# Performance work log

Hardware: AMD Instinct MI355X
Metric: run time of the kernel (lower is better)

## Reference

```python
import jax, jax.numpy as jnp
import numpy as np
from jax import lax

HID = 96              # hidden_dim (C)
DM  = 2 * HID         # SS2D d_model (real+imag interleaved channels)
DI  = 2 * DM          # d_inner (expand=2, VMamba default)
N   = 16              # d_state
K   = 4               # scan directions
R   = (DM + 15) // 16 # dt_rank = ceil(d_model/16)
B_, H_, W_ = 1, 64, 64


def _layernorm(x, w, b, eps=1e-5):
    m = x.mean(-1, keepdims=True)
    v = ((x - m) ** 2).mean(-1, keepdims=True)
    return (x - m) * lax.rsqrt(v + eps) * w + b


def _selective_scan(xs, delta, A, Bs, Cs):
    # xs, delta: (B,K,D,L); A: (K,D,N); Bs, Cs: (B,K,N,L)
    def step(h, inp):
        dt, Bt, Ct, ut = inp                              # (B,K,D),(B,K,N),(B,K,N),(B,K,D)
        dA = jnp.exp(dt[..., None] * A[None])             # (B,K,D,N)
        h = h * dA + dt[..., None] * Bt[:, :, None, :] * ut[..., None]
        y = jnp.einsum('bkdn,bkn->bkd', h, Ct)
        return h, y
    inputs = (jnp.moveaxis(delta, -1, 0), jnp.moveaxis(Bs, -1, 0),
              jnp.moveaxis(Cs, -1, 0), jnp.moveaxis(xs, -1, 0))
    h0 = jnp.zeros(xs.shape[:3] + (N,), xs.dtype)
    _, ys = lax.scan(step, h0, inputs)                    # (L,B,K,D)
    return jnp.moveaxis(ys, 0, -1)                        # (B,K,D,L)


def _forward_core(x, x_proj_w, dt_w, dt_b, A_logs, Ds):
    # x: (B, DI, H, W) -- 4-direction cross-scan (VMamba SS2D)
    B, D, H, W = x.shape
    L = H * W
    x_hw = x.reshape(B, D, L)
    x_wh = x.transpose(0, 1, 3, 2).reshape(B, D, L)
    x_hwwh = jnp.stack([x_hw, x_wh], axis=1)                    # (B,2,D,L)
    xs = jnp.concatenate([x_hwwh, jnp.flip(x_hwwh, -1)], 1)     # (B,4,D,L)
    x_dbl = jnp.einsum('bkdl,kcd->bkcl', xs, x_proj_w)          # (B,K,R+2N,L)
    dts, Bs, Cs = jnp.split(x_dbl, [R, R + N], axis=2)
    dts = jnp.einsum('bkrl,kdr->bkdl', dts, dt_w)
    delta = jax.nn.softplus(dts + dt_b[None, :, :, None])
    A = -jnp.exp(A_logs.reshape(K, D, N))
    ys = _selective_scan(xs, delta, A, Bs, Cs)
    out_y = ys + Ds.reshape(K, D)[None, :, :, None] * xs        # (B,4,D,L)
    inv_y = jnp.flip(out_y[:, 2:4], -1)
    tr = lambda t: t.reshape(B, D, W, H).transpose(0, 1, 3, 2).reshape(B, D, L)
    y = out_y[:, 0] + inv_y[:, 0] + tr(out_y[:, 1]) + tr(inv_y[:, 1])
    return y.transpose(0, 2, 1).reshape(B, H, W, D)


def _ss2d(x, in_proj_w, conv_w, conv_b, x_proj_w, dt_w, dt_b,
          A_logs, Ds, out_norm_w, out_norm_b, out_proj_w):
    # x: (B, H, Wf, DM)
    xz = x @ in_proj_w.T                                        # (B,H,Wf,2*DI)
    xc, z = jnp.split(xz, 2, axis=-1)
    xc = xc.transpose(0, 3, 1, 2)                               # (B,DI,H,Wf)
    xc = lax.conv_general_dilated(xc, conv_w, (1, 1), 'SAME',
                                  feature_group_count=DI,
                                  dimension_numbers=('NCHW', 'OIHW', 'NCHW'))
    xc = jax.nn.silu(xc + conv_b[None, :, None, None])
    y = _forward_core(xc, x_proj_w, dt_w, dt_b, A_logs, Ds)     # (B,H,Wf,DI)
    y = _layernorm(y, out_norm_w, out_norm_b)
    y = y * jax.nn.silu(z)
    return y @ out_proj_w.T                                     # (B,H,Wf,DM)


def _freq_vss(x, in_proj_w, conv_w, conv_b, x_proj_w, dt_w, dt_b,
              A_logs, Ds, out_norm_w, out_norm_b, out_proj_w):
    B, H, W, C = x.shape
    xf = jnp.fft.rfft2(x, axes=(1, 2), norm='ortho')            # (B,H,Wf,C) complex
    Wf = xf.shape[2]
    # interleave real/imag into channels: (B,H,Wf,C,2) -> (B,H,Wf,2C)
    x1 = jnp.stack([xf.real, xf.imag], axis=4).reshape(B, H, Wf, 2 * C)
    att = _ss2d(x1, in_proj_w, conv_w, conv_b, x_proj_w, dt_w, dt_b,
                A_logs, Ds, out_norm_w, out_norm_b, out_proj_w)
    att = att.reshape(B, H, Wf, C, 2)
    attc = lax.complex(att[..., 0], att[..., 1])
    x1r = jnp.fft.irfft2(attc, s=(H, W), axes=(1, 2), norm='ortho')
    return x + x1r                                              # residual (drop_path=0)


def setup_inputs() -> dict:
    key = jax.random.key(0)
    ks = jax.random.split(key, 8)
    s = 0.02
    return {
        'x': jax.random.normal(ks[0], (B_, H_, W_, HID), jnp.float32),
        'in_proj_w': jax.random.normal(ks[1], (2 * DI, DM), jnp.float32) * s,
        'conv_w': jax.random.normal(ks[2], (DI, 1, 3, 3), jnp.float32) * s,
        'conv_b': jnp.zeros((DI,), jnp.float32),
        'x_proj_w': jax.random.normal(ks[3], (K, R + 2 * N, DI), jnp.float32) * s,
        'dt_w': jax.random.normal(ks[4], (K, DI, R), jnp.float32) * s,
        'dt_b': jax.random.normal(ks[5], (K, DI), jnp.float32) * 0.1,
        'A_logs': jnp.tile(jnp.log(jnp.arange(1, N + 1, dtype=jnp.float32))[None], (K * DI, 1)),
        'Ds': jnp.ones((K * DI,), jnp.float32),
        'out_norm_w': jnp.ones((DI,), jnp.float32),
        'out_norm_b': jnp.zeros((DI,), jnp.float32),
        'out_proj_w': jax.random.normal(ks[6], (DM, DI), jnp.float32) * s,
    }


def reference(x, in_proj_w, conv_w, conv_b, x_proj_w, dt_w, dt_b,
              A_logs, Ds, out_norm_w, out_norm_b, out_proj_w):
    return _freq_vss(x, in_proj_w, conv_w, conv_b, x_proj_w, dt_w, dt_b,
                     A_logs, Ds, out_norm_w, out_norm_b, out_proj_w)
```

## Files before the change

### kernel.cpp

```cpp
#include <hip/hip_runtime.h>
#include <hip/hip_bf16.h>

#define LQ   2112
#define DQ   384
#define NST  16
#define HQ   64
#define WFQ  33
#define CQ   96
#define SC   66
#define KDN  24576

#define AX    0
#define AIPW  393216
#define ACW   540672
#define ACB   544128
#define AXPW  544512
#define ADTW  612096
#define ADTB  630528
#define AANEG 632064
#define ADS   656640
#define ANW   658176
#define ANB   658560
#define AOPW  658944
#define ARTOT 732672

#define OFF_FFT   732672
#define OFF_XZ    1138176
#define OFF_XCV   2760192
#define OFF_G     3571200
#define OFF_SUMDT 3942912
#define OFF_HEND  4044288
#define OFF_YS    5666304

#define P_ZR  0
#define P_ZI  202752

static __device__ __forceinline__ float u2f(unsigned short u)
{ union { unsigned int i; float f; } v; v.i = ((unsigned int)u) << 16; return v.f; }

static __device__ __forceinline__ float ldin(const void* p, int o, int isbf)
{
    if (isbf) return u2f(((const unsigned short*)p)[o]);
    return ((const float*)p)[o];
}

static __device__ __forceinline__ int isbf_of(const void* ds)
{ return (((const unsigned int*)ds)[0] == 0x3F803F80u) ? 1 : 0; }

__global__ __launch_bounds__(256) void k_convert_all(
    const void* __restrict__ x,   const void* __restrict__ ipw,
    const void* __restrict__ cw,  const void* __restrict__ cb,
    const void* __restrict__ xpw, const void* __restrict__ dtw,
    const void* __restrict__ dtb, const void* __restrict__ alog,
    const void* __restrict__ ds,  const void* __restrict__ nw,
    const void* __restrict__ nb,  const void* __restrict__ opw,
    float* __restrict__ arena)
{
    int isbf = isbf_of(ds);
    int t = blockIdx.x * 256 + threadIdx.x;
    int o = t;
    if (o < 393216) { arena[t] = ldin(x, o, isbf);   return; }  o -= 393216;
    if (o < 147456) { arena[t] = ldin(ipw, o, isbf); return; }  o -= 147456;
    if (o < 3456)   { arena[t] = ldin(cw, o, isbf);  return; }  o -= 3456;
    if (o < 384)    { arena[t] = ldin(cb, o, isbf);  return; }  o -= 384;
    if (o < 67584)  { arena[t] = ldin(xpw, o, isbf); return; }  o -= 67584;
    if (o < 18432)  { arena[t] = ldin(dtw, o, isbf); return; }  o -= 18432;
    if (o < 1536)   { arena[t] = ldin(dtb, o, isbf); return; }  o -= 1536;
    if (o < 24576)  { arena[t] = -expf(ldin(alog, o, isbf)); return; }  o -= 24576;
    if (o < 1536)   { arena[t] = ldin(ds, o, isbf);  return; }  o -= 1536;
    if (o < 384)    { arena[t] = ldin(nw, o, isbf);  return; }  o -= 384;
    if (o < 384)    { arena[t] = ldin(nb, o, isbf);  return; }  o -= 384;
    arena[t] = ldin(opw, o, isbf);
}

__global__ __launch_bounds__(256) void k_rfftw(const float* __restrict__ x,
                                               float* __restrict__ Zr, float* __restrict__ Zi)
{
    __shared__ float tc[64], ts[64];
    if (threadIdx.x < 64) {
        float ang = -6.283185307179586f * (float)threadIdx.x / 64.f;
        float s, c; __sincosf(ang, &s, &c); tc[threadIdx.x] = c; ts[threadIdx.x] = s;
    }
    __syncthreads();
    int tid = blockIdx.x * 256 + threadIdx.x;
    int c = tid % CQ; int f = (tid / CQ) % WFQ; int h = tid / (CQ * WFQ);
    const float* xp = x + h * 64 * CQ + c;
    float zr = 0.f, zi = 0.f; int j = 0;
    for (int w = 0; w < 64; w++) {
        float xv = xp[w * CQ];
        zr += xv * tc[j]; zi += xv * ts[j];
        j += f; j &= 63;
    }
    Zr[tid] = zr; Zi[tid] = zi;
}

__global__ __launch_bounds__(256) void k_ffth(const float* __restrict__ Zr, const float* __restrict__ Zi,
                                              float* __restrict__ x1)
{
    __shared__ float tc[64], ts[64];
    if (threadIdx.x < 64) {
        float ang = -6.283185307179586f * (float)threadIdx.x / 64.f;
        float s, c; __sincosf(ang, &s, &c); tc[threadIdx.x] = c; ts[threadIdx.x] = s;
    }
    __syncthreads();
    int tid = blockIdx.x * 256 + threadIdx.x;
    int c = tid % CQ; int f = (tid / CQ) % WFQ; int u = tid / (CQ * WFQ);
    float xr = 0.f, xi = 0.f; int j = 0;
    int base = f * CQ + c;
    for (int h = 0; h < 64; h++) {
        float zr = Zr[base + h * (WFQ * CQ)];
        float zi = Zi[base + h * (WFQ * CQ)];
        xr += zr * tc[j] - zi * ts[j];
        xi += zr * ts[j] + zi * tc[j];
        j += u; j &= 63;
    }
    int l = u * WFQ + f;
    x1[l * 192 + 2 * c]     = xr * (1.f / 64.f);
    x1[l * 192 + 2 * c + 1] = xi * (1.f / 64.f);
}

__global__ __launch_bounds__(256) void k_gemm(const float* __restrict__ A, const float* __restrict__ W,
                                              float* __restrict__ C, int N, int K, int sW, int sC)
{
    W += (size_t)blockIdx.z * sW; C += (size_t)blockIdx.z * sC;
    __shared__ float As[16][68];
    __shared__ float Ws[16][68];
    int tid = threadIdx.x;
    int bm = blockIdx.y * 64, bn = blockIdx.x * 64;
    int lr = tid >> 2, lc = (tid & 3) << 2;
    int tx = tid & 15, ty = tid >> 4;
    float acc[4][4] = {};
    for (int k0 = 0; k0 < K; k0 += 16) {
        float4 a4 = *(const float4*)(A + (size_t)(bm + lr) * K + k0 + lc);
        int wrow = bn + lr;
        float4 w4 = make_float4(0.f, 0.f, 0.f, 0.f);
        if (wrow < N) w4 = *(const float4*)(W + (size_t)wrow * K + k0 + lc);
        As[lc][lr] = a4.x; As[lc + 1][lr] = a4.y; As[lc + 2][lr] = a4.z; As[lc + 3][lr] = a4.w;
        Ws[lc][lr] = w4.x; Ws[lc + 1][lr] = w4.y; Ws[lc + 2][lr] = w4.z; Ws[lc + 3][lr] = w4.w;
        __syncthreads();
#pragma unroll
        for (int kk = 0; kk < 16; kk++) {
            float4 av4 = *(const float4*)(&As[kk][ty * 4]);
            float4 wv4 = *(const float4*)(&Ws[kk][tx * 4]);
            float av[4] = {av4.x, av4.y, av4.z, av4.w};
            float wv[4] = {wv4.x, wv4.y, wv4.z, wv4.w};
#pragma unroll
            for (int i = 0; i < 4; i++)
#pragma unroll
                for (int j = 0; j < 4; j++) acc[i][j] += av[i] * wv[j];
        }
        __syncthreads();
    }
#pragma unroll
    for (int i = 0; i < 4; i++) {
        int m = bm + ty * 4 + i;
#pragma unroll
        for (int j = 0; j < 4; j++) {
            int n = bn + tx * 4 + j;
            if (n < N) C[(size_t)m * N + n] = acc[i][j];
        }
    }
}

__global__ __launch_bounds__(256) void k_conv(const float* __restrict__ xz,
                                              const float* __restrict__ ar,
                                              float* __restrict__ xcv)
{
    int tid = blockIdx.x * 256 + threadIdx.x;
    int d = tid % DQ; int l = tid / DQ;
    int h = l / WFQ; int f = l % WFQ;
    float acc = ar[ACB + d];
#pragma unroll
    for (int ky = 0; ky < 3; ky++) {
        int hh = h + ky - 1;
        if (hh < 0 || hh >= HQ) continue;
#pragma unroll
        for (int kx = 0; kx < 3; kx++) {
            int ff = f + kx - 1;
            if (ff < 0 || ff >= WFQ) continue;
            acc += ar[ACW + d * 9 + ky * 3 + kx] * xz[(size_t)(hh * WFQ + ff) * 768 + d];
        }
    }
    float sig = 1.f / (1.f + __expf(-acc));
    xcv[tid] = acc * sig;
}

static __device__ __forceinline__ float softplus_f(float a)
{
    return (a > 15.f) ? a : __logf(1.f + __expf(a));
}

template<int KK> static __device__ __forceinline__ int chunk_l0(int s)
{
    if (KK == 0) return s * 32;
    if (KK == 1) return (s & 1) * 1056 + (s >> 1);
    if (KK == 2) return 2111 - s * 32;
    return 2111 - (s & 1) * 1056 - (s >> 1);
}
template<int KK> static __device__ __forceinline__ int chunk_stp()
{
    if (KK == 0) return 1;
    if (KK == 1) return 33;
    if (KK == 2) return -1;
    return -33;
}

template<int KK, int PASS2> static __device__ __forceinline__ void scan_body(
    const float* __restrict__ xcv, const float* __restrict__ G, const float* __restrict__ ar,
    float* __restrict__ hend, float* __restrict__ sumdt, float* __restrict__ ysum,
    float* __restrict__ dtL, float* __restrict__ duL)
{
    const int s = blockIdx.x, db = blockIdx.y;
    const int lane = threadIdx.x;
    const int d = lane & 15, ng = lane >> 4;
    const int stp = chunk_stp<KK>();
    const int l0 = chunk_l0<KK>(s);
    const float* Gk = G + (size_t)KK * (LQ * 44);

    {
        const int st = lane & 31;
        const int lt = l0 + stp * st;
        const float* gr = Gk + lt * 44;
        float4 g0 = *(const float4*)(gr);
        float4 g1 = *(const float4*)(gr + 4);
        float4 g2 = *(const float4*)(gr + 8);
        const float* ub = xcv + (size_t)lt * DQ + db * 16;
        float uu[16];
        *(float4*)(uu)      = *(const float4*)(ub);
        *(float4*)(uu + 4)  = *(const float4*)(ub + 4);
        *(float4*)(uu + 8)  = *(const float4*)(ub + 8);
        *(float4*)(uu + 12) = *(const float4*)(ub + 12);
#pragma unroll 4
        for (int j = 0; j < 16; j++) {
            const int kdj = KK * DQ + db * 16 + j;
            const float* wp = ar + ADTW + kdj * 12;
            float acc = ar[ADTB + kdj]
                + wp[0] * g0.x + wp[1] * g0.y + wp[2]  * g0.z + wp[3]  * g0.w
                + wp[4] * g1.x + wp[5] * g1.y + wp[6]  * g1.z + wp[7]  * g1.w
                + wp[8] * g2.x + wp[9] * g2.y + wp[10] * g2.z + wp[11] * g2.w;
            float dtv = softplus_f(acc);
            dtL[st * 17 + j] = dtv;
            duL[st * 17 + j] = dtv * uu[j];
        }
    }
    if (!PASS2 && KK == 0 && lane < 32) {
        float4 z4 = make_float4(0.f, 0.f, 0.f, 0.f);
        float* zp = ysum + (size_t)(l0 + lane) * DQ + db * 16;
        *(float4*)zp = z4; *(float4*)(zp + 4) = z4;
        *(float4*)(zp + 8) = z4; *(float4*)(zp + 12) = z4;
    }
    __syncthreads();

    const int kd = KK * DQ + db * 16 + d;
    const int kdn = kd * NST + 4 * ng;
    const float4 Av = *(const float4*)(ar + AANEG + kdn);
    float h0 = 0.f, h1 = 0.f, h2 = 0.f, h3 = 0.f;
    if (PASS2) {
        float4 hh = *(const float4*)(hend + (size_t)s * KDN + kdn);
        h0 = hh.x; h1 = hh.y; h2 = hh.z; h3 = hh.w;
    }

#pragma unroll 4
    for (int i = 0; i < 32; i++) {
        const int l = l0 + stp * i;
        float dt = dtL[i * 17 + d];
        float du = duL[i * 17 + d];
        float4 bv = *(const float4*)(Gk + l * 44 + 12 + 4 * ng);
        h0 = h0 * __expf(dt * Av.x) + du * bv.x;
        h1 = h1 * __expf(dt * Av.y) + du * bv.y;
        h2 = h2 * __expf(dt * Av.z) + du * bv.z;
        h3 = h3 * __expf(dt * Av.w) + du * bv.w;
        if (PASS2) {
            float4 cv = *(const float4*)(Gk + l * 44 + 28 + 4 * ng);
            float yp = h0 * cv.x + h1 * cv.y + h2 * cv.z + h3 * cv.w;
            yp += __shfl_xor(yp, 16);
            yp += __shfl_xor(yp, 32);
            if (ng == 0) atomicAdd(&ysum[(size_t)l * DQ + db * 16 + d], yp);
        }
    }

    if (!PASS2) {
        *(float4*)(hend + (size_t)s * KDN + kdn) = make_float4(h0, h1, h2, h3);
        float sd = 0.f;
#pragma unroll
        for (int t = 0; t < 8; t++) sd += dtL[(ng * 8 + t) * 17 + d];
        sd += __shfl_xor(sd, 16);
        sd += __shfl_xor(sd, 32);
        if (ng == 0) sumdt[s * 1536 + kd] = sd;
    }
}

__global__ __launch_bounds__(64, 8) void k_scan1(const float* __restrict__ xcv, const float* __restrict__ G,
                                                 const float* __restrict__ ar,
                                                 float* __restrict__ hend, float* __restrict__ sumdt,
                                                 float* __restrict__ ysum)
{
    __shared__ float smem[2 * 32 * 17];
    float* dtL = smem; float* duL = smem + 32 * 17;
    switch (blockIdx.z) {
        case 0: scan_body<0, 0>(xcv, G, ar, hend, sumdt, ysum, dtL, duL); break;
        case 1: scan_body<1, 0>(xcv, G, ar, hend, sumdt, ysum, dtL, duL); break;
        case 2: scan_body<2, 0>(xcv, G, ar, hend, sumdt, ysum, dtL, duL); break;
        default: scan_body<3, 0>(xcv, G, ar, hend, sumdt, ysum, dtL, duL); break;
    }
}

__global__ __launch_bounds__(64, 8) void k_scan2(const float* __restrict__ xcv, const float* __restrict__ G,
                                                 const float* __restrict__ ar,
                                                 float* __restrict__ hend, float* __restrict__ sumdt,
                                                 float* __restrict__ ysum)
{
    __shared__ float smem[2 * 32 * 17];
    float* dtL = smem; float* duL = smem + 32 * 17;
    switch (blockIdx.z) {
        case 0: scan_body<0, 1>(xcv, G, ar, hend, sumdt, ysum, dtL, duL); break;
        case 1: scan_body<1, 1>(xcv, G, ar, hend, sumdt, ysum, dtL, duL); break;
        case 2: scan_body<2, 1>(xcv, G, ar, hend, sumdt, ysum, dtL, duL); break;
        default: scan_body<3, 1>(xcv, G, ar, hend, sumdt, ysum, dtL, duL); break;
    }
}

__global__ __launch_bounds__(256) void k_comb(const float* __restrict__ ar, const float* __restrict__ sumdt,
                                              float* __restrict__ hend)
{
    int tid = blockIdx.x * 256 + threadIdx.x;
    int kd = tid >> 4;
    float Av = ar[AANEG + tid];
    float hp = 0.f;
    for (int s = 0; s < SC; s++) {
        float he = hend[(size_t)s * KDN + tid];
        hend[(size_t)s * KDN + tid] = hp;
        hp = hp * __expf(Av * sumdt[s * 1536 + kd]) + he;
    }
}

__global__ __launch_bounds__(128) void k_lnmul(const float* __restrict__ ysum, const float* __restrict__ xcv,
                                               const float* __restrict__ xz, const float* __restrict__ ar,
                                               float* __restrict__ ym)
{
    int l = blockIdx.x; int tid = threadIdx.x;
    float v[3]; float s1 = 0.f, s2 = 0.f;
#pragma unroll
    for (int j = 0; j < 3; j++) {
        int d = tid + j * 128;
        size_t idx = (size_t)l * DQ + d;
        float sd = ar[ADS + d] + ar[ADS + DQ + d] + ar[ADS + 2 * DQ + d] + ar[ADS + 3 * DQ + d];
        float a = ysum[idx] + sd * xcv[idx];
        v[j] = a; s1 += a; s2 += a * a;
    }
#pragma unroll
    for (int off = 1; off < 64; off <<= 1) { s1 += __shfl_xor(s1, off); s2 += __shfl_xor(s2, off); }
    __shared__ float sh[4];
    if ((tid & 63) == 0) { sh[(tid >> 6) * 2] = s1; sh[(tid >> 6) * 2 + 1] = s2; }
    __syncthreads();
    s1 = sh[0] + sh[2]; s2 = sh[1] + sh[3];
    float m = s1 * (1.f / 384.f);
    float var = s2 * (1.f / 384.f) - m * m;
    float rs = rsqrtf(var + 1e-5f);
#pragma unroll
    for (int j = 0; j < 3; j++) {
        int d = tid + j * 128;
        float z = xz[(size_t)l * 768 + 384 + d];
        float sig = 1.f / (1.f + __expf(-z));
        ym[(size_t)l * DQ + d] = ((v[j] - m) * rs * ar[ANW + d] + ar[ANB + d]) * (z * sig);
    }
}

__global__ __launch_bounds__(256) void k_iffth(const float* __restrict__ att,
                                               float* __restrict__ Yr, float* __restrict__ Yi)
{
    __shared__ float tc[64], ts[64];
    if (threadIdx.x < 64) {
        float ang = 6.283185307179586f * (float)threadIdx.x / 64.f;
        float s, c; __sincosf(ang, &s, &c); tc[threadIdx.x] = c; ts[threadIdx.x] = s;
    }
    __syncthreads();
    int tid = blockIdx.x * 256 + threadIdx.x;
    int c = tid % CQ; int f = (tid / CQ) % WFQ; int hp = tid / (CQ * WFQ);
    float yr = 0.f, yi = 0.f; int j = 0;
    for (int h = 0; h < 64; h++) {
        const float* ap = att + (size_t)(h * WFQ + f) * 192 + 2 * c;
        float arv = ap[0], aiv = ap[1];
        yr += arv * tc[j] - aiv * ts[j];
        yi += arv * ts[j] + aiv * tc[j];
        j += hp; j &= 63;
    }
    Yr[tid] = yr * 0.125f;
    Yi[tid] = yi * 0.125f;
}

__global__ __launch_bounds__(256) void k_irfft_res(const float* __restrict__ Yr, const float* __restrict__ Yi,
                                                   const float* __restrict__ x, const void* __restrict__ ds,
                                                   void* __restrict__ out)
{
    __shared__ float tc[64], ts[64];
    if (threadIdx.x < 64) {
        float ang = 6.283185307179586f * (float)threadIdx.x / 64.f;
        float s, c; __sincosf(ang, &s, &c); tc[threadIdx.x] = c; ts[threadIdx.x] = s;
    }
    __syncthreads();
    int tid = blockIdx.x * 256 + threadIdx.x;
    int c = tid % CQ; int w = (tid / CQ) % 64; int h = tid / (CQ * 64);
    const float* yr = Yr + h * (WFQ * CQ) + c;
    const float* yi = Yi + h * (WFQ * CQ) + c;
    float acc = yr[0];
    acc += ((w & 1) ? -1.f : 1.f) * yr[32 * CQ];
    float a2 = 0.f; int j = w & 63;
    for (int f = 1; f < 32; f++) {
        a2 += yr[f * CQ] * tc[j] - yi[f * CQ] * ts[j];
        j += w; j &= 63;
    }
    acc += 2.f * a2;
    float val = x[tid] + 0.125f * acc;
    if (isbf_of(ds)) ((__hip_bfloat16*)out)[tid] = __float2bfloat16(val);
    else             ((float*)out)[tid] = val;
}

extern "C" void kernel_launch(void* const* d_in, const int* in_sizes, int n_in,
                              void* d_out, int out_size, void* d_ws, size_t ws_size,
                              hipStream_t stream)
{
    float* ws    = (float*)d_ws;
    float* ar    = ws;
    float* Zr    = ws + OFF_FFT + P_ZR;
    float* Zi    = ws + OFF_FFT + P_ZI;
    float* xz    = ws + OFF_XZ;
    float* xcv   = ws + OFF_XCV;
    float* G     = ws + OFF_G;
    float* sumdt = ws + OFF_SUMDT;
    float* hend  = ws + OFF_HEND;
    float* YS    = ws + OFF_YS;

    float* x1   = YS;
    float* ysum = YS;
    float* ym   = hend;
    float* att  = xcv;
    float* Yr   = YS;
    float* Yi   = YS + 202752;

    k_convert_all<<<2862, 256, 0, stream>>>(d_in[0], d_in[1], d_in[2], d_in[3], d_in[4], d_in[5],
                                            d_in[6], d_in[7], d_in[8], d_in[9], d_in[10], d_in[11], ar);
    k_rfftw<<<792, 256, 0, stream>>>(ar + AX, Zr, Zi);
    k_ffth<<<792, 256, 0, stream>>>(Zr, Zi, x1);
    k_gemm<<<dim3(12, 33, 1), 256, 0, stream>>>(x1, ar + AIPW, xz, 768, 192, 0, 0);
    k_conv<<<3168, 256, 0, stream>>>(xz, ar, xcv);
    k_gemm<<<dim3(1, 33, 4), 256, 0, stream>>>(xcv, ar + AXPW, G, 44, 384, 44 * 384, LQ * 44);
    k_scan1<<<dim3(SC, 24, 4), 64, 0, stream>>>(xcv, G, ar, hend, sumdt, ysum);
    k_comb<<<96, 256, 0, stream>>>(ar, sumdt, hend);
    k_scan2<<<dim3(SC, 24, 4), 64, 0, stream>>>(xcv, G, ar, hend, sumdt, ysum);
    k_lnmul<<<LQ, 128, 0, stream>>>(ysum, xcv, xz, ar, ym);
    k_gemm<<<dim3(3, 33, 1), 256, 0, stream>>>(ym, ar + AOPW, att, 192, 384, 0, 0);
    k_iffth<<<792, 256, 0, stream>>>(att, Yr, Yi);
    k_irfft_res<<<1536, 256, 0, stream>>>(Yr, Yi, ar + AX, d_in[8], d_out);
}
```

Measured before the change: 249.4 us.

## Fuse 2D forward and inverse FFT passes into single kernels via shared memory

Merges the W-direction rFFT and H-direction FFT into one kernel per (frequency column, 4-channel group), keeping the intermediate spectrum in shared memory. The H-direction inverse FFT and the inverse real FFT plus residual are merged the same way. This removes two launches and the global round trips of the intermediate Zr/Zi and Yr/Yi buffers. In exchange, the first pass of each fused kernel recomputes the column transform per block with narrow 4-channel accesses, which may coalesce poorly, and the inverse kernel leaves about half its threads idle in the first phase.

Result: slower. 261.5 us (+4.8%).

```diff
diff --git a/kernel.cpp b/kernel.cpp
--- a/kernel.cpp
+++ b/kernel.cpp
@@ -24,16 +24,13 @@
 #define AOPW  658944
 #define ARTOT 732672
 
-#define OFF_FFT   732672
+#define OFF_X1    732672
 #define OFF_XZ    1138176
 #define OFF_XCV   2760192
 #define OFF_G     3571200
 #define OFF_SUMDT 3942912
 #define OFF_HEND  4044288
 #define OFF_YS    5666304
-
-#define P_ZR  0
-#define P_ZI  202752
 
 static __device__ __forceinline__ float u2f(unsigned short u)
 { union { unsigned int i; float f; } v; v.i = ((unsigned int)u) << 16; return v.f; }
@@ -73,50 +70,42 @@
     arena[t] = ldin(opw, o, isbf);
 }
 
-__global__ __launch_bounds__(256) void k_rfftw(const float* __restrict__ x,
-                                               float* __restrict__ Zr, float* __restrict__ Zi)
+__global__ __launch_bounds__(256) void k_rfft2(const float* __restrict__ x, float* __restrict__ x1)
 {
     __shared__ float tc[64], ts[64];
+    __shared__ float Zr[64][4], Zi[64][4];
     if (threadIdx.x < 64) {
         float ang = -6.283185307179586f * (float)threadIdx.x / 64.f;
         float s, c; __sincosf(ang, &s, &c); tc[threadIdx.x] = c; ts[threadIdx.x] = s;
     }
     __syncthreads();
-    int tid = blockIdx.x * 256 + threadIdx.x;
-    int c = tid % CQ; int f = (tid / CQ) % WFQ; int h = tid / (CQ * WFQ);
-    const float* xp = x + h * 64 * CQ + c;
-    float zr = 0.f, zi = 0.f; int j = 0;
-    for (int w = 0; w < 64; w++) {
-        float xv = xp[w * CQ];
-        zr += xv * tc[j]; zi += xv * ts[j];
-        j += f; j &= 63;
-    }
-    Zr[tid] = zr; Zi[tid] = zi;
-}
-
-__global__ __launch_bounds__(256) void k_ffth(const float* __restrict__ Zr, const float* __restrict__ Zi,
-                                              float* __restrict__ x1)
-{
-    __shared__ float tc[64], ts[64];
-    if (threadIdx.x < 64) {
-        float ang = -6.283185307179586f * (float)threadIdx.x / 64.f;
-        float s, c; __sincosf(ang, &s, &c); tc[threadIdx.x] = c; ts[threadIdx.x] = s;
-    }
-    __syncthreads();
-    int tid = blockIdx.x * 256 + threadIdx.x;
-    int c = tid % CQ; int f = (tid / CQ) % WFQ; int u = tid / (CQ * WFQ);
-    float xr = 0.f, xi = 0.f; int j = 0;
-    int base = f * CQ + c;
-    for (int h = 0; h < 64; h++) {
-        float zr = Zr[base + h * (WFQ * CQ)];
-        float zi = Zi[base + h * (WFQ * CQ)];
-        xr += zr * tc[j] - zi * ts[j];
-        xi += zr * ts[j] + zi * tc[j];
-        j += u; j &= 63;
-    }
-    int l = u * WFQ + f;
-    x1[l * 192 + 2 * c]     = xr * (1.f / 64.f);
-    x1[l * 192 + 2 * c + 1] = xi * (1.f / 64.f);
+    const int f = blockIdx.x;
+    const int cc = threadIdx.x & 3;
+    const int c = blockIdx.y * 4 + cc;
+    {
+        const int h = threadIdx.x >> 2;
+        const float* xp = x + h * (64 * CQ) + c;
+        float zr = 0.f, zi = 0.f; int j = 0;
+        for (int w = 0; w < 64; w++) {
+            float xv = xp[w * CQ];
+            zr += xv * tc[j]; zi += xv * ts[j];
+            j += f; j &= 63;
+        }
+        Zr[h][cc] = zr; Zi[h][cc] = zi;
+    }
+    __syncthreads();
+    {
+        const int u = threadIdx.x >> 2;
+        float xr = 0.f, xi = 0.f; int j = 0;
+        for (int h = 0; h < 64; h++) {
+            float zr = Zr[h][cc], zi = Zi[h][cc];
+            xr += zr * tc[j] - zi * ts[j];
+            xi += zr * ts[j] + zi * tc[j];
+            j += u; j &= 63;
+        }
+        const int l = u * WFQ + f;
+        *(float2*)(x1 + (size_t)l * 192 + 2 * c) = make_float2(xr * (1.f / 64.f), xi * (1.f / 64.f));
+    }
 }
 
 __global__ __launch_bounds__(256) void k_gemm(const float* __restrict__ A, const float* __restrict__ W,
@@ -366,54 +355,47 @@
     }
 }
 
-__global__ __launch_bounds__(256) void k_iffth(const float* __restrict__ att,
-                                               float* __restrict__ Yr, float* __restrict__ Yi)
+__global__ __launch_bounds__(256) void k_irfft2(const float* __restrict__ att,
+                                                const float* __restrict__ x, const void* __restrict__ ds,
+                                                void* __restrict__ out)
 {
     __shared__ float tc[64], ts[64];
+    __shared__ float Yr[33][4], Yi[33][4];
     if (threadIdx.x < 64) {
         float ang = 6.283185307179586f * (float)threadIdx.x / 64.f;
         float s, c; __sincosf(ang, &s, &c); tc[threadIdx.x] = c; ts[threadIdx.x] = s;
     }
     __syncthreads();
-    int tid = blockIdx.x * 256 + threadIdx.x;
-    int c = tid % CQ; int f = (tid / CQ) % WFQ; int hp = tid / (CQ * WFQ);
-    float yr = 0.f, yi = 0.f; int j = 0;
-    for (int h = 0; h < 64; h++) {
-        const float* ap = att + (size_t)(h * WFQ + f) * 192 + 2 * c;
-        float arv = ap[0], aiv = ap[1];
-        yr += arv * tc[j] - aiv * ts[j];
-        yi += arv * ts[j] + aiv * tc[j];
-        j += hp; j &= 63;
-    }
-    Yr[tid] = yr * 0.125f;
-    Yi[tid] = yi * 0.125f;
-}
-
-__global__ __launch_bounds__(256) void k_irfft_res(const float* __restrict__ Yr, const float* __restrict__ Yi,
-                                                   const float* __restrict__ x, const void* __restrict__ ds,
-                                                   void* __restrict__ out)
-{
-    __shared__ float tc[64], ts[64];
-    if (threadIdx.x < 64) {
-        float ang = 6.283185307179586f * (float)threadIdx.x / 64.f;
-        float s, c; __sincosf(ang, &s, &c); tc[threadIdx.x] = c; ts[threadIdx.x] = s;
-    }
-    __syncthreads();
-    int tid = blockIdx.x * 256 + threadIdx.x;
-    int c = tid % CQ; int w = (tid / CQ) % 64; int h = tid / (CQ * 64);
-    const float* yr = Yr + h * (WFQ * CQ) + c;
-    const float* yi = Yi + h * (WFQ * CQ) + c;
-    float acc = yr[0];
-    acc += ((w & 1) ? -1.f : 1.f) * yr[32 * CQ];
-    float a2 = 0.f; int j = w & 63;
-    for (int f = 1; f < 32; f++) {
-        a2 += yr[f * CQ] * tc[j] - yi[f * CQ] * ts[j];
-        j += w; j &= 63;
-    }
-    acc += 2.f * a2;
-    float val = x[tid] + 0.125f * acc;
-    if (isbf_of(ds)) ((__hip_bfloat16*)out)[tid] = __float2bfloat16(val);
-    else             ((float*)out)[tid] = val;
+    const int hp = blockIdx.x;
+    const int cb = blockIdx.y * 4;
+    if (threadIdx.x < 132) {
+        const int f = threadIdx.x >> 2, cc = threadIdx.x & 3;
+        const float* ap = att + (size_t)f * 192 + 2 * (cb + cc);
+        float yr = 0.f, yi = 0.f; int j = 0;
+        for (int h = 0; h < 64; h++) {
+            float2 a2 = *(const float2*)(ap + (size_t)h * (WFQ * 192));
+            yr += a2.x * tc[j] - a2.y * ts[j];
+            yi += a2.x * ts[j] + a2.y * tc[j];
+            j += hp; j &= 63;
+        }
+        Yr[f][cc] = yr; Yi[f][cc] = yi;
+    }
+    __syncthreads();
+    {
+        const int w = threadIdx.x >> 2, cc = threadIdx.x & 3;
+        const int c = cb + cc;
+        float acc = Yr[0][cc] + ((w & 1) ? -1.f : 1.f) * Yr[32][cc];
+        float a2 = 0.f; int j = w;
+        for (int f = 1; f < 32; f++) {
+            a2 += Yr[f][cc] * tc[j] - Yi[f][cc] * ts[j];
+            j += w; j &= 63;
+        }
+        acc += 2.f * a2;
+        const int o = (hp * 64 + w) * CQ + c;
+        float val = x[o] + acc * (1.f / 64.f);
+        if (isbf_of(ds)) ((__hip_bfloat16*)out)[o] = __float2bfloat16(val);
+        else             ((float*)out)[o] = val;
+    }
 }
 
 extern "C" void kernel_launch(void* const* d_in, const int* in_sizes, int n_in,
@@ -422,26 +404,20 @@
 {
     float* ws    = (float*)d_ws;
     float* ar    = ws;
-    float* Zr    = ws + OFF_FFT + P_ZR;
-    float* Zi    = ws + OFF_FFT + P_ZI;
+    float* x1    = ws + OFF_X1;
     float* xz    = ws + OFF_XZ;
     float* xcv   = ws + OFF_XCV;
     float* G     = ws + OFF_G;
     float* sumdt = ws + OFF_SUMDT;
     float* hend  = ws + OFF_HEND;
-    float* YS    = ws + OFF_YS;
-
-    float* x1   = YS;
-    float* ysum = YS;
+    float* ysum  = ws + OFF_YS;
+
     float* ym   = hend;
     float* att  = xcv;
-    float* Yr   = YS;
-    float* Yi   = YS + 202752;
 
     k_convert_all<<<2862, 256, 0, stream>>>(d_in[0], d_in[1], d_in[2], d_in[3], d_in[4], d_in[5],
                                             d_in[6], d_in[7], d_in[8], d_in[9], d_in[10], d_in[11], ar);
-    k_rfftw<<<792, 256, 0, stream>>>(ar + AX, Zr, Zi);
-    k_ffth<<<792, 256, 0, stream>>>(Zr, Zi, x1);
+    k_rfft2<<<dim3(33, 24), 256, 0, stream>>>(ar + AX, x1);
     k_gemm<<<dim3(12, 33, 1), 256, 0, stream>>>(x1, ar + AIPW, xz, 768, 192, 0, 0);
     k_conv<<<3168, 256, 0, stream>>>(xz, ar, xcv);
     k_gemm<<<dim3(1, 33, 4), 256, 0, stream>>>(xcv, ar + AXPW, G, 44, 384, 44 * 384, LQ * 44);
@@ -450,6 +426,5 @@
     k_scan2<<<dim3(SC, 24, 4), 64, 0, stream>>>(xcv, G, ar, hend, sumdt, ysum);
     k_lnmul<<<LQ, 128, 0, stream>>>(ysum, xcv, xz, ar, ym);
     k_gemm<<<dim3(3, 33, 1), 256, 0, stream>>>(ym, ar + AOPW, att, 192, 384, 0, 0);
-    k_iffth<<<792, 256, 0, stream>>>(att, Yr, Yi);
-    k_irfft_res<<<1536, 256, 0, stream>>>(Yr, Yi, ar + AX, d_in[8], d_out);
-}
+    k_irfft2<<<dim3(64, 24), 256, 0, stream>>>(att, ar + AX, d_in[8], d_out);
+}
```
